# Kernel optimization log

Measured on AMD Instinct MI355X. Metric: run time of the kernel, lower is better.

Reference implementation:

```python
import jax, jax.numpy as jnp
import numpy as np

# Static config (matches init_kwargs)
B, H, W, C = 16, 64, 64, 512
HEADS, WS, SHIFT = 16, 8, 4
N = WS * WS                      # tokens per window = 64
NW = (H // WS) * (W // WS)       # windows per image = 64
HID = 4 * C                      # MLP hidden = 2048
HEAD_DIM = C // HEADS
SCALE = HEAD_DIM ** -0.5
EPS = 1e-5


def _layer_norm(x, w, b):
    m = jnp.mean(x, axis=-1, keepdims=True)
    v = jnp.mean((x - m) ** 2, axis=-1, keepdims=True)
    return (x - m) / jnp.sqrt(v + EPS) * w + b


def _rel_pos_idx():
    coords = np.stack(np.meshgrid(np.arange(WS), np.arange(WS), indexing='ij')).reshape(2, -1)
    rel = coords[:, :, None] - coords[:, None, :]          # (2, N, N)
    rel = rel.transpose(1, 2, 0)                           # (N, N, 2)
    rel[:, :, 0] += WS - 1
    rel[:, :, 1] += WS - 1
    rel[:, :, 0] *= 2 * WS - 1
    return rel.sum(-1)                                     # (N, N) int


def _attn_mask():
    img = np.zeros((H, W), dtype=np.float32)
    sls = (slice(0, -WS), slice(-WS, -SHIFT), slice(-SHIFT, None))
    cnt = 0
    for hs in sls:
        for ws_ in sls:
            img[hs, ws_] = cnt
            cnt += 1
    # window partition (H,W) -> (NW, N)
    mw = img.reshape(H // WS, WS, W // WS, WS).transpose(0, 2, 1, 3).reshape(-1, N)
    diff = mw[:, None, :] - mw[:, :, None]                 # (NW, N, N)
    return np.where(diff != 0, -100.0, 0.0).astype(np.float32)


def setup_inputs() -> dict:
    key = jax.random.key(0)
    ks = jax.random.split(key, 8)
    s = 0.02
    return {
        'x': jax.random.normal(ks[0], (B, H * W, C), jnp.float32),
        'qkv_w': jax.random.normal(ks[1], (3 * C, C), jnp.float32) * s,
        'qkv_b': jnp.zeros((3 * C,), jnp.float32),
        'proj_w': jax.random.normal(ks[2], (C, C), jnp.float32) * s,
        'proj_b': jnp.zeros((C,), jnp.float32),
        'norm1_w': jnp.ones((C,), jnp.float32),
        'norm1_b': jnp.zeros((C,), jnp.float32),
        'norm2_w': jnp.ones((C,), jnp.float32),
        'norm2_b': jnp.zeros((C,), jnp.float32),
        'fc1_w': jax.random.normal(ks[3], (HID, C), jnp.float32) * s,
        'fc1_b': jnp.zeros((HID,), jnp.float32),
        'fc2_w': jax.random.normal(ks[4], (C, HID), jnp.float32) * s,
        'fc2_b': jnp.zeros((C,), jnp.float32),
        'rel_bias_table': jax.random.normal(ks[5], ((2 * WS - 1) ** 2, HEADS), jnp.float32) * s,
        'rel_pos_idx': jnp.asarray(_rel_pos_idx(), jnp.int32),
        'attn_mask': jnp.asarray(_attn_mask(), jnp.float32),
    }


def _swin_block(x, qkv_w, qkv_b, proj_w, proj_b, norm1_w, norm1_b,
                norm2_w, norm2_b, fc1_w, fc1_b, fc2_w, fc2_b,
                rel_bias_table, rel_pos_idx, attn_mask):
    Bx = x.shape[0]
    shortcut = x
    h = _layer_norm(x, norm1_w, norm1_b).reshape(Bx, H, W, C)
    h = jnp.roll(h, (-SHIFT, -SHIFT), axis=(1, 2))
    # window partition -> (B*NW, N, C)
    h = h.reshape(Bx, H // WS, WS, W // WS, WS, C).transpose(0, 1, 3, 2, 4, 5)
    h = h.reshape(Bx * NW, N, C)
    # qkv projection
    qkv = h @ qkv_w.T + qkv_b                               # (B_, N, 3C)
    qkv = qkv.reshape(Bx * NW, N, 3, HEADS, HEAD_DIM).transpose(2, 0, 3, 1, 4)
    q, k, v = qkv[0], qkv[1], qkv[2]                        # (B_, heads, N, hd)
    attn = jnp.einsum('bhnd,bhmd->bhnm', q, k) * SCALE      # (B_, heads, N, N)
    rp_bias = rel_bias_table[rel_pos_idx]                   # (N, N, heads)
    attn = attn + rp_bias.transpose(2, 0, 1)[None]
    # shift mask (per window)
    attn = attn.reshape(Bx, NW, HEADS, N, N) + attn_mask[None, :, None]
    attn = jax.nn.softmax(attn.reshape(Bx * NW, HEADS, N, N), axis=-1)
    o = jnp.einsum('bhnm,bhmd->bhnd', attn, v)              # (B_, heads, N, hd)
    o = o.transpose(0, 2, 1, 3).reshape(Bx * NW, N, C)
    o = o @ proj_w.T + proj_b
    # window reverse -> (B, H, W, C)
    o = o.reshape(Bx, H // WS, W // WS, WS, WS, C).transpose(0, 1, 3, 2, 4, 5)
    o = o.reshape(Bx, H, W, C)
    o = jnp.roll(o, (SHIFT, SHIFT), axis=(1, 2))
    x = shortcut + o.reshape(Bx, H * W, C)
    # MLP
    h2 = _layer_norm(x, norm2_w, norm2_b)
    h2 = jax.nn.gelu(h2 @ fc1_w.T + fc1_b, approximate=False)
    return x + (h2 @ fc2_w.T + fc2_b)


def reference(x, qkv_w, qkv_b, proj_w, proj_b, norm1_w, norm1_b,
              norm2_w, norm2_b, fc1_w, fc1_b, fc2_w, fc2_b,
              rel_bias_table, rel_pos_idx, attn_mask):
    return _swin_block(x, qkv_w, qkv_b, proj_w, proj_b, norm1_w, norm1_b,
                       norm2_w, norm2_b, fc1_w, fc1_b, fc2_w, fc2_b,
                       rel_bias_table, rel_pos_idx, attn_mask)
```

## Files before the change

kernel.cpp:

```cpp
#include <hip/hip_runtime.h>
#include <hip/hip_bf16.h>

typedef __attribute__((ext_vector_type(8))) short short8;
typedef __attribute__((ext_vector_type(4))) float f32x4;

__device__ __forceinline__ short f2bfbits(float f) {
  union { __hip_bfloat16 h; short s; } cvt;
  cvt.h = __float2bfloat16(f);
  return cvt.s;
}
__device__ __forceinline__ float bfbits2f(short bits) {
  union { unsigned int u; float f; } cvt;
  cvt.u = ((unsigned int)(unsigned short)bits) << 16;
  return cvt.f;
}

__device__ __forceinline__ void gl_lds16(const short* g, short* l) {
  __builtin_amdgcn_global_load_lds(
      (__attribute__((address_space(1))) void*)(g),
      (__attribute__((address_space(3))) void*)(l), 16, 0, 0);
}

__global__ __launch_bounds__(256)
void f2bf(const float* __restrict__ s, short* __restrict__ d, int n) {
  const int i = (blockIdx.x * 256 + threadIdx.x) * 4;
  if (i >= n) return;
  float4 v = *(const float4*)(s + i);
  short o[4] = {f2bfbits(v.x), f2bfbits(v.y), f2bfbits(v.z), f2bfbits(v.w)};
  *(uint2*)(d + i) = *(const uint2*)o;
}

__global__ __launch_bounds__(256)
void bm_build(const float* __restrict__ table, const int* __restrict__ idx,
              const float* __restrict__ mask, short* __restrict__ bm) {
  const int wi = blockIdx.x, hh = blockIdx.y;
  const int n = threadIdx.x & 63;
  const int m0 = (threadIdx.x >> 6) * 16;
#pragma unroll
  for (int mm = 0; mm < 16; mm++) {
    const int m = m0 + mm;
    const float t = table[idx[m * 64 + n] * 16 + hh];
    const float mk = mask[wi * 4096 + m * 64 + n];
    bm[((long)(wi * 16 + hh) * 64 + m) * 64 + n] = f2bfbits(t + mk);
  }
}

__global__ __launch_bounds__(256)
void ln1_win(const float* __restrict__ x, const float* __restrict__ w,
             const float* __restrict__ b, short* __restrict__ h) {
  const int lane = threadIdx.x & 63;
  const int wv = threadIdx.x >> 6;
  const int t = blockIdx.x * 4 + wv;
  const int n = t & 63, wiB = t >> 6;
  const int wi = wiB & 63, bb = wiB >> 6;
  const int sr = (((wi >> 3) << 3) + (n >> 3) + 4) & 63;
  const int sc = (((wi & 7) << 3) + (n & 7) + 4) & 63;
  const float* xp = x + ((long)bb * 4096 + sr * 64 + sc) * 512 + lane * 8;
  float4 u0 = *(const float4*)(xp);
  float4 u1 = *(const float4*)(xp + 4);
  float v[8] = {u0.x, u0.y, u0.z, u0.w, u1.x, u1.y, u1.z, u1.w};
  float s = 0.f;
#pragma unroll
  for (int j = 0; j < 8; j++) s += v[j];
#pragma unroll
  for (int o = 1; o < 64; o <<= 1) s += __shfl_xor(s, o, 64);
  const float mean = s * (1.0f / 512.0f);
  float q = 0.f;
#pragma unroll
  for (int j = 0; j < 8; j++) { float d = v[j] - mean; q += d * d; }
#pragma unroll
  for (int o = 1; o < 64; o <<= 1) q += __shfl_xor(q, o, 64);
  const float rstd = rsqrtf(q * (1.0f / 512.0f) + 1e-5f);
  float4 w0 = *(const float4*)(w + lane * 8);
  float4 w1 = *(const float4*)(w + lane * 8 + 4);
  float4 b0 = *(const float4*)(b + lane * 8);
  float4 b1 = *(const float4*)(b + lane * 8 + 4);
  const float wv8[8] = {w0.x, w0.y, w0.z, w0.w, w1.x, w1.y, w1.z, w1.w};
  const float bv8[8] = {b0.x, b0.y, b0.z, b0.w, b1.x, b1.y, b1.z, b1.w};
  short outs[8];
#pragma unroll
  for (int j = 0; j < 8; j++)
    outs[j] = f2bfbits((v[j] - mean) * rstd * wv8[j] + bv8[j]);
  *(uint4*)(h + (long)t * 512 + lane * 8) = *(const uint4*)outs;
}

__global__ __launch_bounds__(256)
void ln2_id(const float* __restrict__ x2, const float* __restrict__ w,
            const float* __restrict__ b, short* __restrict__ out) {
  const int lane = threadIdx.x & 63;
  const int wv = threadIdx.x >> 6;
  const long t = blockIdx.x * 4 + wv;
  const float* xp = x2 + t * 512 + lane * 8;
  float4 u0 = *(const float4*)(xp);
  float4 u1 = *(const float4*)(xp + 4);
  float v[8] = {u0.x, u0.y, u0.z, u0.w, u1.x, u1.y, u1.z, u1.w};
  float s = 0.f;
#pragma unroll
  for (int j = 0; j < 8; j++) s += v[j];
#pragma unroll
  for (int o = 1; o < 64; o <<= 1) s += __shfl_xor(s, o, 64);
  const float mean = s * (1.0f / 512.0f);
  float q = 0.f;
#pragma unroll
  for (int j = 0; j < 8; j++) { float d = v[j] - mean; q += d * d; }
#pragma unroll
  for (int o = 1; o < 64; o <<= 1) q += __shfl_xor(q, o, 64);
  const float rstd = rsqrtf(q * (1.0f / 512.0f) + 1e-5f);
  float4 w0 = *(const float4*)(w + lane * 8);
  float4 w1 = *(const float4*)(w + lane * 8 + 4);
  float4 b0 = *(const float4*)(b + lane * 8);
  float4 b1 = *(const float4*)(b + lane * 8 + 4);
  const float wv8[8] = {w0.x, w0.y, w0.z, w0.w, w1.x, w1.y, w1.z, w1.w};
  const float bv8[8] = {b0.x, b0.y, b0.z, b0.w, b1.x, b1.y, b1.z, b1.w};
  short outs[8];
#pragma unroll
  for (int j = 0; j < 8; j++)
    outs[j] = f2bfbits((v[j] - mean) * rstd * wv8[j] + bv8[j]);
  *(uint4*)(out + t * 512 + lane * 8) = *(const uint4*)outs;
}

template <int MODE, int K, int GN>
__global__ __launch_bounds__(512, 2)
void gemm256(const short* __restrict__ A, const short* __restrict__ Bw,
             const float* __restrict__ bias, const float* __restrict__ aux,
             void* __restrict__ outv, short* __restrict__ out2) {
  __shared__ short lds[65536];
  constexpr int NT = K / 64;
  const int tid = threadIdx.x;
  const int lane = tid & 63, wave = tid >> 6;
  const int l15 = lane & 15, quad = lane >> 4;
  const int wr = wave >> 2, wc = wave & 3;

  const int nwg = gridDim.x;
  const int chunk = nwg >> 3;
  const int wg = (blockIdx.x & 7) * chunk + (blockIdx.x >> 3);
  const int row0 = (wg / GN) * 256;
  const int col0 = (wg % GN) * 256;

  const int srow = lane >> 3;
  const int scol = ((lane & 7) ^ srow) * 8;
  const short* Ag = A + (long)(row0 + wave * 8 + srow) * K + scol;
  const short* Bg = Bw + (long)(col0 + wave * 8 + srow) * K + scol;
  short* ldsAw = lds + wave * 512;
  short* ldsBw = lds + 32768 + wave * 512;

  const int g0 = (quad ^ (l15 & 7)) * 8;
  const int g1 = ((quad ^ 4) ^ (l15 & 7)) * 8;
  const int aB0 = (wr * 128 + l15) * 64 + g0;
  const int aB1 = (wr * 128 + l15) * 64 + g1;
  const int bB0 = 32768 + (wc * 64 + l15) * 64 + g0;
  const int bB1 = 32768 + (wc * 64 + l15) * 64 + g1;

  f32x4 acc[8][4];
#pragma unroll
  for (int m = 0; m < 8; m++)
#pragma unroll
    for (int n = 0; n < 4; n++) acc[m][n] = (f32x4){0.f, 0.f, 0.f, 0.f};

#define STAGE(cOff, kt)                                               \
  {                                                                   \
    const short* a_ = Ag + (kt) * 64;                                 \
    const short* b_ = Bg + (kt) * 64;                                 \
    _Pragma("unroll") for (int i_ = 0; i_ < 4; i_++) {                \
      gl_lds16(a_ + (long)i_ * 64 * K, ldsAw + (cOff) + i_ * 4096);   \
      gl_lds16(b_ + (long)i_ * 64 * K, ldsBw + (cOff) + i_ * 4096);   \
    }                                                                 \
  }

  STAGE(0, 0);
  STAGE(16384, 1);
  asm volatile("s_waitcnt vmcnt(8)" ::: "memory");
  __builtin_amdgcn_s_barrier();

  for (int t = 0; t < NT; ++t) {
    const int c = (t & 1) << 14;
    const short* pa0 = lds + c + aB0;
    const short* pa1 = lds + c + aB1;
    const short* pb0 = lds + c + bB0;
    const short* pb1 = lds + c + bB1;
    short8 B0[4], B1[4], A0[4], A1[4], A2[4], A3[4];

#pragma unroll
    for (int n = 0; n < 4; n++) B0[n] = *(const short8*)(pb0 + n * 1024);
#pragma unroll
    for (int m = 0; m < 4; m++) A0[m] = *(const short8*)(pa0 + m * 1024);
    asm volatile("" ::: "memory");
    __builtin_amdgcn_s_barrier();
    __builtin_amdgcn_s_setprio(1);
#pragma unroll
    for (int m = 0; m < 4; m++)
#pragma unroll
      for (int n = 0; n < 4; n++)
        acc[m][n] = __builtin_amdgcn_mfma_f32_16x16x32_bf16(A0[m], B0[n], acc[m][n], 0, 0, 0);
    __builtin_amdgcn_s_setprio(0);
    __builtin_amdgcn_s_barrier();

#pragma unroll
    for (int m = 0; m < 4; m++) A1[m] = *(const short8*)(pa0 + (m + 4) * 1024);
#pragma unroll
    for (int n = 0; n < 4; n++) B1[n] = *(const short8*)(pb1 + n * 1024);
    asm volatile("" ::: "memory");
    __builtin_amdgcn_s_barrier();
    __builtin_amdgcn_s_setprio(1);
#pragma unroll
    for (int m = 0; m < 4; m++)
#pragma unroll
      for (int n = 0; n < 4; n++)
        acc[m + 4][n] = __builtin_amdgcn_mfma_f32_16x16x32_bf16(A1[m], B0[n], acc[m + 4][n], 0, 0, 0);
    __builtin_amdgcn_s_setprio(0);
    __builtin_amdgcn_s_barrier();

#pragma unroll
    for (int m = 0; m < 4; m++) A2[m] = *(const short8*)(pa1 + m * 1024);
#pragma unroll
    for (int m = 0; m < 4; m++) A3[m] = *(const short8*)(pa1 + (m + 4) * 1024);
    asm volatile("" ::: "memory");
    __builtin_amdgcn_s_barrier();
    __builtin_amdgcn_s_setprio(1);
#pragma unroll
    for (int m = 0; m < 4; m++)
#pragma unroll
      for (int n = 0; n < 4; n++)
        acc[m][n] = __builtin_amdgcn_mfma_f32_16x16x32_bf16(A2[m], B1[n], acc[m][n], 0, 0, 0);
    __builtin_amdgcn_s_setprio(0);
    asm volatile("s_waitcnt lgkmcnt(0)" ::: "memory");
    __builtin_amdgcn_s_barrier();

    if (t + 2 < NT) STAGE(c, t + 2);
    __builtin_amdgcn_s_barrier();
    __builtin_amdgcn_s_setprio(1);
#pragma unroll
    for (int m = 0; m < 4; m++)
#pragma unroll
      for (int n = 0; n < 4; n++)
        acc[m + 4][n] = __builtin_amdgcn_mfma_f32_16x16x32_bf16(A3[m], B1[n], acc[m + 4][n], 0, 0, 0);
    __builtin_amdgcn_s_setprio(0);
    if (t + 2 < NT) {
      asm volatile("s_waitcnt vmcnt(8)" ::: "memory");
    } else if (t + 1 < NT) {
      asm volatile("s_waitcnt vmcnt(0)" ::: "memory");
    }
    __builtin_amdgcn_s_barrier();
  }
#undef STAGE

  const int rW = row0 + wr * 128;
  const int cW = col0 + wc * 64;
  if constexpr (MODE == 0) {
    if (col0 >= 1024) {
#pragma unroll
      for (int m = 0; m < 8; m++) {
        const int rbase = rW + m * 16 + quad * 4;
        const int w_ = rbase >> 6, tokb = rbase & 63;
#pragma unroll
        for (int n = 0; n < 4; n++) {
          const int col = cW + n * 16 + l15;
          const float bv = bias[col];
          const int cg = col - 1024;
          const int head = cg >> 5, d = cg & 31;
          short pk[4];
#pragma unroll
          for (int r = 0; r < 4; r++) pk[r] = f2bfbits(acc[m][n][r] + bv);
          *(uint2*)(out2 + ((long)(w_ * 16 + head) * 32 + d) * 64 + tokb) = *(const uint2*)pk;
        }
      }
    } else {
#pragma unroll
      for (int m = 0; m < 8; m++)
#pragma unroll
        for (int n = 0; n < 4; n++) {
          const int col = cW + n * 16 + l15;
          const float bv = bias[col];
#pragma unroll
          for (int r = 0; r < 4; r++) {
            const int row = rW + m * 16 + quad * 4 + r;
            ((short*)outv)[(long)row * 1024 + col] = f2bfbits(acc[m][n][r] + bv);
          }
        }
    }
  } else {
#pragma unroll
    for (int m = 0; m < 8; m++)
#pragma unroll
      for (int n = 0; n < 4; n++) {
        const int col = cW + n * 16 + l15;
        const float bv = bias[col];
#pragma unroll
        for (int r = 0; r < 4; r++) {
          const int row = rW + m * 16 + quad * 4 + r;
          float v = acc[m][n][r] + bv;
          if constexpr (MODE == 1) {
            const int n_ = row & 63, wiB = row >> 6;
            const int wi = wiB & 63, bb = wiB >> 6;
            const int p = (((wi >> 3) << 3) + (n_ >> 3) + 4) & 63;
            const int qq = (((wi & 7) << 3) + (n_ & 7) + 4) & 63;
            const long dst = ((long)bb * 4096 + p * 64 + qq) * 512 + col;
            ((float*)outv)[dst] = v + aux[dst];
          } else if constexpr (MODE == 2) {
            const float g = 0.5f * v * (1.0f + erff(v * 0.70710678118654752f));
            ((short*)outv)[(long)row * (GN * 256) + col] = f2bfbits(g);
          } else {
            const long ix = (long)row * (GN * 256) + col;
            ((float*)outv)[ix] = v + aux[ix];
          }
        }
      }
  }
}

__global__ __launch_bounds__(256)
void attn(const short* __restrict__ qk, const short* __restrict__ vT,
          const short* __restrict__ bm, short* __restrict__ o) {
  __shared__ short P[4][64 * 72];
  const int lane = threadIdx.x & 63, wave = threadIdx.x >> 6;
  const int l15 = lane & 15, quad = lane >> 4;
  const int w = blockIdx.x;
  const int hh = blockIdx.y * 4 + wave;
  const int wi = w & 63;
  const short* base = qk + (long)w * 64 * 1024;

  short8 qf[4], kf[4];
#pragma unroll
  for (int mt = 0; mt < 4; mt++) {
    const int tq = mt * 16 + l15;
    qf[mt] = *(const short8*)(base + tq * 1024 + hh * 32 + quad * 8);
    kf[mt] = *(const short8*)(base + tq * 1024 + 512 + hh * 32 + quad * 8);
  }
  f32x4 S[4][4];
#pragma unroll
  for (int i = 0; i < 4; i++)
#pragma unroll
    for (int j = 0; j < 4; j++) S[i][j] = (f32x4){0.f, 0.f, 0.f, 0.f};
#pragma unroll
  for (int mt = 0; mt < 4; mt++)
#pragma unroll
    for (int nt = 0; nt < 4; nt++)
      S[mt][nt] = __builtin_amdgcn_mfma_f32_16x16x32_bf16(qf[mt], kf[nt], S[mt][nt], 0, 0, 0);

  short* pw = P[wave];
  const short* bmp = bm + (long)(wi * 16 + hh) * 4096;
  const float scale = 0.17677669529663687f;
#pragma unroll
  for (int mt = 0; mt < 4; mt++) {
#pragma unroll
    for (int reg = 0; reg < 4; reg++) {
      const int m = mt * 16 + quad * 4 + reg;
      float vals[4];
#pragma unroll
      for (int nt = 0; nt < 4; nt++)
        vals[nt] = S[mt][nt][reg] * scale + bfbits2f(bmp[m * 64 + nt * 16 + l15]);
      float mx = fmaxf(fmaxf(vals[0], vals[1]), fmaxf(vals[2], vals[3]));
#pragma unroll
      for (int o_ = 1; o_ < 16; o_ <<= 1) mx = fmaxf(mx, __shfl_xor(mx, o_, 64));
      float e[4], sum = 0.f;
#pragma unroll
      for (int nt = 0; nt < 4; nt++) { e[nt] = __expf(vals[nt] - mx); sum += e[nt]; }
#pragma unroll
      for (int o_ = 1; o_ < 16; o_ <<= 1) sum += __shfl_xor(sum, o_, 64);
      const float inv = 1.0f / sum;
#pragma unroll
      for (int nt = 0; nt < 4; nt++)
        pw[m * 72 + nt * 16 + l15] = f2bfbits(e[nt] * inv);
    }
  }
  __syncthreads();

  const short* vbase = vT + (long)(w * 16 + hh) * 2048;
  f32x4 O[4][2];
#pragma unroll
  for (int i = 0; i < 4; i++)
#pragma unroll
    for (int j = 0; j < 2; j++) O[i][j] = (f32x4){0.f, 0.f, 0.f, 0.f};
#pragma unroll
  for (int ks = 0; ks < 2; ks++) {
    short8 vf[2];
#pragma unroll
    for (int nt = 0; nt < 2; nt++)
      vf[nt] = *(const short8*)(vbase + (nt * 16 + l15) * 64 + ks * 32 + quad * 8);
#pragma unroll
    for (int mt = 0; mt < 4; mt++) {
      short8 pf = *(const short8*)(pw + (mt * 16 + l15) * 72 + ks * 32 + quad * 8);
#pragma unroll
      for (int nt = 0; nt < 2; nt++)
        O[mt][nt] = __builtin_amdgcn_mfma_f32_16x16x32_bf16(pf, vf[nt], O[mt][nt], 0, 0, 0);
    }
  }
#pragma unroll
  for (int mt = 0; mt < 4; mt++)
#pragma unroll
    for (int nt = 0; nt < 2; nt++)
#pragma unroll
      for (int reg = 0; reg < 4; reg++) {
        const int t = mt * 16 + quad * 4 + reg;
        const int d = nt * 16 + l15;
        o[((long)w * 64 + t) * 512 + hh * 32 + d] = f2bfbits(O[mt][nt][reg]);
      }
}

extern "C" void kernel_launch(void* const* d_in, const int* in_sizes, int n_in,
                              void* d_out, int out_size, void* d_ws, size_t ws_size,
                              hipStream_t stream) {
  const float* x      = (const float*)d_in[0];
  const float* qkv_w  = (const float*)d_in[1];
  const float* qkv_b  = (const float*)d_in[2];
  const float* proj_w = (const float*)d_in[3];
  const float* proj_b = (const float*)d_in[4];
  const float* n1w    = (const float*)d_in[5];
  const float* n1b    = (const float*)d_in[6];
  const float* n2w    = (const float*)d_in[7];
  const float* n2b    = (const float*)d_in[8];
  const float* fc1_w  = (const float*)d_in[9];
  const float* fc1_b  = (const float*)d_in[10];
  const float* fc2_w  = (const float*)d_in[11];
  const float* fc2_b  = (const float*)d_in[12];
  const float* table  = (const float*)d_in[13];
  const int*   idx    = (const int*)d_in[14];
  const float* mask   = (const float*)d_in[15];

  char* ws = (char*)d_ws;
  const long MB = 1048576L;
  short* wq  = (short*)(ws);
  short* wp  = wq + 786432;
  short* w1  = wp + 262144;
  short* w2  = w1 + 1048576;
  short* bm  = (short*)(ws + 8 * MB);
  short* h   = (short*)(ws + 17 * MB);
  short* o   = h;
  short* xn2 = h;
  short* qk  = (short*)(ws + 81 * MB);
  short* h2c = qk;
  short* vT  = (short*)(ws + 209 * MB);
  float* out = (float*)d_out;

  f2bf<<<768, 256, 0, stream>>>(qkv_w, wq, 786432);
  f2bf<<<256, 256, 0, stream>>>(proj_w, wp, 262144);
  f2bf<<<1024, 256, 0, stream>>>(fc1_w, w1, 1048576);
  f2bf<<<1024, 256, 0, stream>>>(fc2_w, w2, 1048576);
  bm_build<<<dim3(64, 16), 256, 0, stream>>>(table, idx, mask, bm);

  ln1_win<<<16384, 256, 0, stream>>>(x, n1w, n1b, h);
  gemm256<0, 512, 6><<<1536, 512, 0, stream>>>(h, wq, qkv_b, nullptr, qk, vT);
  attn<<<dim3(1024, 4), 256, 0, stream>>>(qk, vT, bm, o);
  gemm256<1, 512, 2><<<512, 512, 0, stream>>>(o, wp, proj_b, x, out, nullptr);
  ln2_id<<<16384, 256, 0, stream>>>(out, n2w, n2b, xn2);
  for (int c = 0; c < 2; c++) {
    const long ro = (long)c * 32768;
    gemm256<2, 512, 8><<<1024, 512, 0, stream>>>(
        xn2 + ro * 512, w1, fc1_b, nullptr, h2c, nullptr);
    gemm256<3, 2048, 2><<<256, 512, 0, stream>>>(
        h2c, w2, fc2_b, out + ro * 512, out + ro * 512, nullptr);
  }
}
```

Measured before the change: 1.006 ms.

## Loop GEMM blocks over multiple M tiles and drop a redundant attention barrier

Adds an MTB template parameter so each GEMM workgroup processes several consecutive 256-row tiles in one continuous K pipeline. The epilogue now runs inside the loop while the next tile's first stages are already prefetched, and the grids shrink to match. The intent is to amortize pipeline prologue and epilogue cost and to overlap output stores with loads. The risk is that the smaller grids (768, 256 and 256 blocks) leave compute units idle or unbalanced at two blocks per CU. Separately, the attention kernel drops the __syncthreads after writing each wave's private P buffer, relying on intra-wave ordering.

```diff
diff --git a/kernel.cpp b/kernel.cpp
--- a/kernel.cpp
+++ b/kernel.cpp
@@ -119,13 +119,15 @@
   *(uint4*)(out + t * 512 + lane * 8) = *(const uint4*)outs;
 }
 
-template <int MODE, int K, int GN>
+template <int MODE, int K, int GN, int MTB>
 __global__ __launch_bounds__(512, 2)
 void gemm256(const short* __restrict__ A, const short* __restrict__ Bw,
              const float* __restrict__ bias, const float* __restrict__ aux,
              void* __restrict__ outv, short* __restrict__ out2) {
   __shared__ short lds[65536];
   constexpr int NT = K / 64;
+  constexpr int LNT = (NT == 8) ? 3 : (NT == 16 ? 4 : 5);
+  constexpr int TOT = MTB * NT;
   const int tid = threadIdx.x;
   const int lane = tid & 63, wave = tid >> 6;
   const int l15 = lane & 15, quad = lane >> 4;
@@ -134,7 +136,7 @@
   const int nwg = gridDim.x;
   const int chunk = nwg >> 3;
   const int wg = (blockIdx.x & 7) * chunk + (blockIdx.x >> 3);
-  const int row0 = (wg / GN) * 256;
+  const int row0 = (wg / GN) * (256 * MTB);
   const int col0 = (wg % GN) * 256;
 
   const int srow = lane >> 3;
@@ -157,14 +159,15 @@
 #pragma unroll
     for (int n = 0; n < 4; n++) acc[m][n] = (f32x4){0.f, 0.f, 0.f, 0.f};
 
-#define STAGE(cOff, kt)                                               \
-  {                                                                   \
-    const short* a_ = Ag + (kt) * 64;                                 \
-    const short* b_ = Bg + (kt) * 64;                                 \
-    _Pragma("unroll") for (int i_ = 0; i_ < 4; i_++) {                \
-      gl_lds16(a_ + (long)i_ * 64 * K, ldsAw + (cOff) + i_ * 4096);   \
-      gl_lds16(b_ + (long)i_ * 64 * K, ldsBw + (cOff) + i_ * 4096);   \
-    }                                                                 \
+#define STAGE(cOff, kt)                                                     \
+  {                                                                         \
+    const short* a_ = Ag + (long)((kt) >> LNT) * (256 * K) +                \
+                      ((kt) & (NT - 1)) * 64;                               \
+    const short* b_ = Bg + ((kt) & (NT - 1)) * 64;                          \
+    _Pragma("unroll") for (int i_ = 0; i_ < 4; i_++) {                      \
+      gl_lds16(a_ + (long)i_ * 64 * K, ldsAw + (cOff) + i_ * 4096);         \
+      gl_lds16(b_ + (long)i_ * 64 * K, ldsBw + (cOff) + i_ * 4096);         \
+    }                                                                       \
   }
 
   STAGE(0, 0);
@@ -172,7 +175,7 @@
   asm volatile("s_waitcnt vmcnt(8)" ::: "memory");
   __builtin_amdgcn_s_barrier();
 
-  for (int t = 0; t < NT; ++t) {
+  for (int t = 0; t < TOT; ++t) {
     const int c = (t & 1) << 14;
     const short* pa0 = lds + c + aB0;
     const short* pa1 = lds + c + aB1;
@@ -226,7 +229,7 @@
     asm volatile("s_waitcnt lgkmcnt(0)" ::: "memory");
     __builtin_amdgcn_s_barrier();
 
-    if (t + 2 < NT) STAGE(c, t + 2);
+    if (t + 2 < TOT) STAGE(c, t + 2);
     __builtin_amdgcn_s_barrier();
     __builtin_amdgcn_s_setprio(1);
 #pragma unroll
@@ -235,77 +238,86 @@
       for (int n = 0; n < 4; n++)
         acc[m + 4][n] = __builtin_amdgcn_mfma_f32_16x16x32_bf16(A3[m], B1[n], acc[m + 4][n], 0, 0, 0);
     __builtin_amdgcn_s_setprio(0);
-    if (t + 2 < NT) {
+    if (t + 2 < TOT) {
       asm volatile("s_waitcnt vmcnt(8)" ::: "memory");
-    } else if (t + 1 < NT) {
+    } else if (t + 1 < TOT) {
       asm volatile("s_waitcnt vmcnt(0)" ::: "memory");
     }
     __builtin_amdgcn_s_barrier();
+
+    if ((t & (NT - 1)) == NT - 1) {
+      const int rW = row0 + (t >> LNT) * 256 + wr * 128;
+      const int cW = col0 + wc * 64;
+      if constexpr (MODE == 0) {
+        if (col0 >= 1024) {
+#pragma unroll
+          for (int m = 0; m < 8; m++) {
+            const int rbase = rW + m * 16 + quad * 4;
+            const int w_ = rbase >> 6, tokb = rbase & 63;
+#pragma unroll
+            for (int n = 0; n < 4; n++) {
+              const int col = cW + n * 16 + l15;
+              const float bv = bias[col];
+              const int cg = col - 1024;
+              const int head = cg >> 5, d = cg & 31;
+              short pk[4];
+#pragma unroll
+              for (int r = 0; r < 4; r++) pk[r] = f2bfbits(acc[m][n][r] + bv);
+              *(uint2*)(out2 + ((long)(w_ * 16 + head) * 32 + d) * 64 + tokb) =
+                  *(const uint2*)pk;
+            }
+          }
+        } else {
+#pragma unroll
+          for (int m = 0; m < 8; m++)
+#pragma unroll
+            for (int n = 0; n < 4; n++) {
+              const int col = cW + n * 16 + l15;
+              const float bv = bias[col];
+#pragma unroll
+              for (int r = 0; r < 4; r++) {
+                const int row = rW + m * 16 + quad * 4 + r;
+                ((short*)outv)[(long)row * 1024 + col] = f2bfbits(acc[m][n][r] + bv);
+              }
+            }
+        }
+      } else {
+#pragma unroll
+        for (int m = 0; m < 8; m++)
+#pragma unroll
+          for (int n = 0; n < 4; n++) {
+            const int col = cW + n * 16 + l15;
+            const float bv = bias[col];
+#pragma unroll
+            for (int r = 0; r < 4; r++) {
+              const int row = rW + m * 16 + quad * 4 + r;
+              float v = acc[m][n][r] + bv;
+              if constexpr (MODE == 1) {
+                const int n_ = row & 63, wiB = row >> 6;
+                const int wi = wiB & 63, bb = wiB >> 6;
+                const int p = (((wi >> 3) << 3) + (n_ >> 3) + 4) & 63;
+                const int qq = (((wi & 7) << 3) + (n_ & 7) + 4) & 63;
+                const long dst = ((long)bb * 4096 + p * 64 + qq) * 512 + col;
+                ((float*)outv)[dst] = v + aux[dst];
+              } else if constexpr (MODE == 2) {
+                const float g = 0.5f * v * (1.0f + erff(v * 0.70710678118654752f));
+                ((short*)outv)[(long)row * (GN * 256) + col] = f2bfbits(g);
+              } else {
+                const long ix = (long)row * (GN * 256) + col;
+                ((float*)outv)[ix] = v + aux[ix];
+              }
+            }
+          }
+      }
+      if (t + 1 < TOT) {
+#pragma unroll
+        for (int m = 0; m < 8; m++)
+#pragma unroll
+          for (int n = 0; n < 4; n++) acc[m][n] = (f32x4){0.f, 0.f, 0.f, 0.f};
+      }
+    }
   }
 #undef STAGE
-
-  const int rW = row0 + wr * 128;
-  const int cW = col0 + wc * 64;
-  if constexpr (MODE == 0) {
-    if (col0 >= 1024) {
-#pragma unroll
-      for (int m = 0; m < 8; m++) {
-        const int rbase = rW + m * 16 + quad * 4;
-        const int w_ = rbase >> 6, tokb = rbase & 63;
-#pragma unroll
-        for (int n = 0; n < 4; n++) {
-          const int col = cW + n * 16 + l15;
-          const float bv = bias[col];
-          const int cg = col - 1024;
-          const int head = cg >> 5, d = cg & 31;
-          short pk[4];
-#pragma unroll
-          for (int r = 0; r < 4; r++) pk[r] = f2bfbits(acc[m][n][r] + bv);
-          *(uint2*)(out2 + ((long)(w_ * 16 + head) * 32 + d) * 64 + tokb) = *(const uint2*)pk;
-        }
-      }
-    } else {
-#pragma unroll
-      for (int m = 0; m < 8; m++)
-#pragma unroll
-        for (int n = 0; n < 4; n++) {
-          const int col = cW + n * 16 + l15;
-          const float bv = bias[col];
-#pragma unroll
-          for (int r = 0; r < 4; r++) {
-            const int row = rW + m * 16 + quad * 4 + r;
-            ((short*)outv)[(long)row * 1024 + col] = f2bfbits(acc[m][n][r] + bv);
-          }
-        }
-    }
-  } else {
-#pragma unroll
-    for (int m = 0; m < 8; m++)
-#pragma unroll
-      for (int n = 0; n < 4; n++) {
-        const int col = cW + n * 16 + l15;
-        const float bv = bias[col];
-#pragma unroll
-        for (int r = 0; r < 4; r++) {
-          const int row = rW + m * 16 + quad * 4 + r;
-          float v = acc[m][n][r] + bv;
-          if constexpr (MODE == 1) {
-            const int n_ = row & 63, wiB = row >> 6;
-            const int wi = wiB & 63, bb = wiB >> 6;
-            const int p = (((wi >> 3) << 3) + (n_ >> 3) + 4) & 63;
-            const int qq = (((wi & 7) << 3) + (n_ & 7) + 4) & 63;
-            const long dst = ((long)bb * 4096 + p * 64 + qq) * 512 + col;
-            ((float*)outv)[dst] = v + aux[dst];
-          } else if constexpr (MODE == 2) {
-            const float g = 0.5f * v * (1.0f + erff(v * 0.70710678118654752f));
-            ((short*)outv)[(long)row * (GN * 256) + col] = f2bfbits(g);
-          } else {
-            const long ix = (long)row * (GN * 256) + col;
-            ((float*)outv)[ix] = v + aux[ix];
-          }
-        }
-      }
-  }
 }
 
 __global__ __launch_bounds__(256)
@@ -363,7 +375,6 @@
         pw[m * 72 + nt * 16 + l15] = f2bfbits(e[nt] * inv);
     }
   }
-  __syncthreads();
 
   const short* vbase = vT + (long)(w * 16 + hh) * 2048;
   f32x4 O[4][2];
@@ -439,15 +450,15 @@
   bm_build<<<dim3(64, 16), 256, 0, stream>>>(table, idx, mask, bm);
 
   ln1_win<<<16384, 256, 0, stream>>>(x, n1w, n1b, h);
-  gemm256<0, 512, 6><<<1536, 512, 0, stream>>>(h, wq, qkv_b, nullptr, qk, vT);
+  gemm256<0, 512, 6, 2><<<768, 512, 0, stream>>>(h, wq, qkv_b, nullptr, qk, vT);
   attn<<<dim3(1024, 4), 256, 0, stream>>>(qk, vT, bm, o);
-  gemm256<1, 512, 2><<<512, 512, 0, stream>>>(o, wp, proj_b, x, out, nullptr);
+  gemm256<1, 512, 2, 2><<<256, 512, 0, stream>>>(o, wp, proj_b, x, out, nullptr);
   ln2_id<<<16384, 256, 0, stream>>>(out, n2w, n2b, xn2);
   for (int c = 0; c < 2; c++) {
     const long ro = (long)c * 32768;
-    gemm256<2, 512, 8><<<1024, 512, 0, stream>>>(
+    gemm256<2, 512, 8, 4><<<256, 512, 0, stream>>>(
         xn2 + ro * 512, w1, fc1_b, nullptr, h2c, nullptr);
-    gemm256<3, 2048, 2><<<256, 512, 0, stream>>>(
+    gemm256<3, 2048, 2, 1><<<256, 512, 0, stream>>>(
         h2c, w2, fc2_b, out + ro * 512, out + ro * 512, nullptr);
   }
 }
```

Measured after the change: 1.105 ms. +9.8%, slower.

## Shrink GEMM tiles from 256x256 to 128x128 with 4-wave workgroups

Applied to the files above, without the earlier changes.

Replaces the 256x256-tile, 8-wave GEMM with a 128x128-tile, 4-wave version that uses half the LDS and a simpler two-phase MFMA loop with fewer barriers. Launch grids grow by 4x, which gives more workgroups for load balance and occupancy but lowers data reuse per tile. The attention kernel also drops the __syncthreads after writing P. Each wave writes and reads only its own P slice, so this is likely safe, but it removes an explicit ordering point.

```diff
diff --git a/kernel.cpp b/kernel.cpp
--- a/kernel.cpp
+++ b/kernel.cpp
@@ -120,40 +120,40 @@
 }
 
 template <int MODE, int K, int GN>
-__global__ __launch_bounds__(512, 2)
-void gemm256(const short* __restrict__ A, const short* __restrict__ Bw,
+__global__ __launch_bounds__(256, 2)
+void gemm128(const short* __restrict__ A, const short* __restrict__ Bw,
              const float* __restrict__ bias, const float* __restrict__ aux,
              void* __restrict__ outv, short* __restrict__ out2) {
-  __shared__ short lds[65536];
+  __shared__ short lds[32768];
   constexpr int NT = K / 64;
   const int tid = threadIdx.x;
   const int lane = tid & 63, wave = tid >> 6;
   const int l15 = lane & 15, quad = lane >> 4;
-  const int wr = wave >> 2, wc = wave & 3;
+  const int wr = wave >> 1, wc = wave & 1;
 
   const int nwg = gridDim.x;
   const int chunk = nwg >> 3;
   const int wg = (blockIdx.x & 7) * chunk + (blockIdx.x >> 3);
-  const int row0 = (wg / GN) * 256;
-  const int col0 = (wg % GN) * 256;
+  const int row0 = (wg / GN) * 128;
+  const int col0 = (wg % GN) * 128;
 
   const int srow = lane >> 3;
   const int scol = ((lane & 7) ^ srow) * 8;
-  const short* Ag = A + (long)(row0 + wave * 8 + srow) * K + scol;
-  const short* Bg = Bw + (long)(col0 + wave * 8 + srow) * K + scol;
-  short* ldsAw = lds + wave * 512;
-  short* ldsBw = lds + 32768 + wave * 512;
+  const short* Ag = A + (long)(row0 + wave * 32 + srow) * K + scol;
+  const short* Bg = Bw + (long)(col0 + wave * 32 + srow) * K + scol;
+  short* ldsAw = lds + wave * 2048;
+  short* ldsBw = lds + 16384 + wave * 2048;
 
   const int g0 = (quad ^ (l15 & 7)) * 8;
   const int g1 = ((quad ^ 4) ^ (l15 & 7)) * 8;
-  const int aB0 = (wr * 128 + l15) * 64 + g0;
-  const int aB1 = (wr * 128 + l15) * 64 + g1;
-  const int bB0 = 32768 + (wc * 64 + l15) * 64 + g0;
-  const int bB1 = 32768 + (wc * 64 + l15) * 64 + g1;
-
-  f32x4 acc[8][4];
-#pragma unroll
-  for (int m = 0; m < 8; m++)
+  const int aB0 = (wr * 64 + l15) * 64 + g0;
+  const int aB1 = (wr * 64 + l15) * 64 + g1;
+  const int bB0 = 16384 + (wc * 64 + l15) * 64 + g0;
+  const int bB1 = 16384 + (wc * 64 + l15) * 64 + g1;
+
+  f32x4 acc[4][4];
+#pragma unroll
+  for (int m = 0; m < 4; m++)
 #pragma unroll
     for (int n = 0; n < 4; n++) acc[m][n] = (f32x4){0.f, 0.f, 0.f, 0.f};
 
@@ -162,23 +162,23 @@
     const short* a_ = Ag + (kt) * 64;                                 \
     const short* b_ = Bg + (kt) * 64;                                 \
     _Pragma("unroll") for (int i_ = 0; i_ < 4; i_++) {                \
-      gl_lds16(a_ + (long)i_ * 64 * K, ldsAw + (cOff) + i_ * 4096);   \
-      gl_lds16(b_ + (long)i_ * 64 * K, ldsBw + (cOff) + i_ * 4096);   \
+      gl_lds16(a_ + (long)i_ * 8 * K, ldsAw + (cOff) + i_ * 512);     \
+      gl_lds16(b_ + (long)i_ * 8 * K, ldsBw + (cOff) + i_ * 512);     \
     }                                                                 \
   }
 
   STAGE(0, 0);
-  STAGE(16384, 1);
+  STAGE(8192, 1);
   asm volatile("s_waitcnt vmcnt(8)" ::: "memory");
   __builtin_amdgcn_s_barrier();
 
   for (int t = 0; t < NT; ++t) {
-    const int c = (t & 1) << 14;
+    const int c = (t & 1) << 13;
     const short* pa0 = lds + c + aB0;
     const short* pa1 = lds + c + aB1;
     const short* pb0 = lds + c + bB0;
     const short* pb1 = lds + c + bB1;
-    short8 B0[4], B1[4], A0[4], A1[4], A2[4], A3[4];
+    short8 A0[4], A1[4], B0[4], B1[4];
 
 #pragma unroll
     for (int n = 0; n < 4; n++) B0[n] = *(const short8*)(pb0 + n * 1024);
@@ -196,44 +196,18 @@
     __builtin_amdgcn_s_barrier();
 
 #pragma unroll
-    for (int m = 0; m < 4; m++) A1[m] = *(const short8*)(pa0 + (m + 4) * 1024);
+    for (int m = 0; m < 4; m++) A1[m] = *(const short8*)(pa1 + m * 1024);
 #pragma unroll
     for (int n = 0; n < 4; n++) B1[n] = *(const short8*)(pb1 + n * 1024);
-    asm volatile("" ::: "memory");
-    __builtin_amdgcn_s_barrier();
-    __builtin_amdgcn_s_setprio(1);
-#pragma unroll
-    for (int m = 0; m < 4; m++)
-#pragma unroll
-      for (int n = 0; n < 4; n++)
-        acc[m + 4][n] = __builtin_amdgcn_mfma_f32_16x16x32_bf16(A1[m], B0[n], acc[m + 4][n], 0, 0, 0);
-    __builtin_amdgcn_s_setprio(0);
-    __builtin_amdgcn_s_barrier();
-
-#pragma unroll
-    for (int m = 0; m < 4; m++) A2[m] = *(const short8*)(pa1 + m * 1024);
-#pragma unroll
-    for (int m = 0; m < 4; m++) A3[m] = *(const short8*)(pa1 + (m + 4) * 1024);
-    asm volatile("" ::: "memory");
-    __builtin_amdgcn_s_barrier();
-    __builtin_amdgcn_s_setprio(1);
-#pragma unroll
-    for (int m = 0; m < 4; m++)
-#pragma unroll
-      for (int n = 0; n < 4; n++)
-        acc[m][n] = __builtin_amdgcn_mfma_f32_16x16x32_bf16(A2[m], B1[n], acc[m][n], 0, 0, 0);
-    __builtin_amdgcn_s_setprio(0);
     asm volatile("s_waitcnt lgkmcnt(0)" ::: "memory");
     __builtin_amdgcn_s_barrier();
-
     if (t + 2 < NT) STAGE(c, t + 2);
-    __builtin_amdgcn_s_barrier();
     __builtin_amdgcn_s_setprio(1);
 #pragma unroll
     for (int m = 0; m < 4; m++)
 #pragma unroll
       for (int n = 0; n < 4; n++)
-        acc[m + 4][n] = __builtin_amdgcn_mfma_f32_16x16x32_bf16(A3[m], B1[n], acc[m + 4][n], 0, 0, 0);
+        acc[m][n] = __builtin_amdgcn_mfma_f32_16x16x32_bf16(A1[m], B1[n], acc[m][n], 0, 0, 0);
     __builtin_amdgcn_s_setprio(0);
     if (t + 2 < NT) {
       asm volatile("s_waitcnt vmcnt(8)" ::: "memory");
@@ -244,12 +218,12 @@
   }
 #undef STAGE
 
-  const int rW = row0 + wr * 128;
+  const int rW = row0 + wr * 64;
   const int cW = col0 + wc * 64;
   if constexpr (MODE == 0) {
     if (col0 >= 1024) {
 #pragma unroll
-      for (int m = 0; m < 8; m++) {
+      for (int m = 0; m < 4; m++) {
         const int rbase = rW + m * 16 + quad * 4;
         const int w_ = rbase >> 6, tokb = rbase & 63;
 #pragma unroll
@@ -261,12 +235,13 @@
           short pk[4];
 #pragma unroll
           for (int r = 0; r < 4; r++) pk[r] = f2bfbits(acc[m][n][r] + bv);
-          *(uint2*)(out2 + ((long)(w_ * 16 + head) * 32 + d) * 64 + tokb) = *(const uint2*)pk;
+          *(uint2*)(out2 + ((long)(w_ * 16 + head) * 32 + d) * 64 + tokb) =
+              *(const uint2*)pk;
         }
       }
     } else {
 #pragma unroll
-      for (int m = 0; m < 8; m++)
+      for (int m = 0; m < 4; m++)
 #pragma unroll
         for (int n = 0; n < 4; n++) {
           const int col = cW + n * 16 + l15;
@@ -280,7 +255,7 @@
     }
   } else {
 #pragma unroll
-    for (int m = 0; m < 8; m++)
+    for (int m = 0; m < 4; m++)
 #pragma unroll
       for (int n = 0; n < 4; n++) {
         const int col = cW + n * 16 + l15;
@@ -298,9 +273,9 @@
             ((float*)outv)[dst] = v + aux[dst];
           } else if constexpr (MODE == 2) {
             const float g = 0.5f * v * (1.0f + erff(v * 0.70710678118654752f));
-            ((short*)outv)[(long)row * (GN * 256) + col] = f2bfbits(g);
+            ((short*)outv)[(long)row * (GN * 128) + col] = f2bfbits(g);
           } else {
-            const long ix = (long)row * (GN * 256) + col;
+            const long ix = (long)row * (GN * 128) + col;
             ((float*)outv)[ix] = v + aux[ix];
           }
         }
@@ -363,7 +338,6 @@
         pw[m * 72 + nt * 16 + l15] = f2bfbits(e[nt] * inv);
     }
   }
-  __syncthreads();
 
   const short* vbase = vT + (long)(w * 16 + hh) * 2048;
   f32x4 O[4][2];
@@ -439,15 +413,15 @@
   bm_build<<<dim3(64, 16), 256, 0, stream>>>(table, idx, mask, bm);
 
   ln1_win<<<16384, 256, 0, stream>>>(x, n1w, n1b, h);
-  gemm256<0, 512, 6><<<1536, 512, 0, stream>>>(h, wq, qkv_b, nullptr, qk, vT);
+  gemm128<0, 512, 12><<<6144, 256, 0, stream>>>(h, wq, qkv_b, nullptr, qk, vT);
   attn<<<dim3(1024, 4), 256, 0, stream>>>(qk, vT, bm, o);
-  gemm256<1, 512, 2><<<512, 512, 0, stream>>>(o, wp, proj_b, x, out, nullptr);
+  gemm128<1, 512, 4><<<2048, 256, 0, stream>>>(o, wp, proj_b, x, out, nullptr);
   ln2_id<<<16384, 256, 0, stream>>>(out, n2w, n2b, xn2);
   for (int c = 0; c < 2; c++) {
     const long ro = (long)c * 32768;
-    gemm256<2, 512, 8><<<1024, 512, 0, stream>>>(
+    gemm128<2, 512, 16><<<4096, 256, 0, stream>>>(
         xn2 + ro * 512, w1, fc1_b, nullptr, h2c, nullptr);
-    gemm256<3, 2048, 2><<<256, 512, 0, stream>>>(
+    gemm128<3, 2048, 4><<<1024, 256, 0, stream>>>(
         h2c, w2, fc2_b, out + ro * 512, out + ro * 512, nullptr);
   }
 }
```

After: 991.1 us. No clear change (-1.5%).
